# Optimization experiments

Hardware: AMD Instinct MI355X
Metric: run time of the kernel (lower is better)

## Reference

```python
import jax, jax.numpy as jnp
import numpy as np
from jax import lax

DIM = 96
B, S = 2, 48
EPS_LN = 1e-6
EPS_GRN = 1e-6


def setup_inputs() -> dict:
    key = jax.random.key(0)
    ks = jax.random.split(key, 11)
    d, h = DIM, 4 * DIM
    return {
        "x": jax.random.normal(ks[0], (B, d, S, S, S), jnp.float32),
        "dw_w": jax.random.normal(ks[1], (d, 1, 7, 7, 7), jnp.float32) * 0.05,  # (O, I/groups, kD,kH,kW)
        "dw_b": jax.random.normal(ks[2], (d,), jnp.float32) * 0.02,
        "ln_w": jnp.ones((d,), jnp.float32),
        "ln_b": jnp.zeros((d,), jnp.float32),
        "w1": jax.random.normal(ks[3], (d, h), jnp.float32) * 0.02,
        "b1": jax.random.normal(ks[4], (h,), jnp.float32) * 0.02,
        "grn_w": jax.random.normal(ks[5], (h,), jnp.float32) * 0.02,
        "grn_b": jax.random.normal(ks[6], (h,), jnp.float32) * 0.02,
        "w2": jax.random.normal(ks[7], (h, d), jnp.float32) * 0.02,
        "b2": jax.random.normal(ks[8], (d,), jnp.float32) * 0.02,
    }


def reference(x, dw_w, dw_b, ln_w, ln_b, w1, b1, grn_w, grn_b, w2, b2):
    # depthwise 7x7x7 conv, padding 3, groups = channels; x: (B, C, D, H, W)
    y = lax.conv_general_dilated(
        x, dw_w, window_strides=(1, 1, 1), padding=[(3, 3)] * 3,
        dimension_numbers=("NCDHW", "OIDHW", "NCDHW"), feature_group_count=DIM,
    ) + dw_b[None, :, None, None, None]
    # channels_last: (B, D, H, W, C)
    h = jnp.transpose(y, (0, 2, 3, 4, 1))
    # LayerNorm over channel dim
    mu = jnp.mean(h, axis=-1, keepdims=True)
    var = jnp.mean((h - mu) ** 2, axis=-1, keepdims=True)
    h = (h - mu) * lax.rsqrt(var + EPS_LN) * ln_w + ln_b
    # pointwise MLP expand + GELU (exact, erf-based, like torch)
    h = jnp.einsum("bdhwc,ce->bdhwe", h, w1) + b1
    h = jax.nn.gelu(h, approximate=False)
    # GRN: global L2 norm over spatial dims (1,2,3), per channel
    g = jnp.sqrt(jnp.sum(h * h, axis=(1, 2, 3), keepdims=True))  # (B,1,1,1,4C)
    n = g / (jnp.mean(g, axis=-1, keepdims=True) + EPS_GRN)
    h = grn_w * (h * n) + grn_b + h
    # pointwise MLP contract
    h = jnp.einsum("bdhwe,ec->bdhwc", h, w2) + b2
    # back to channels_first + residual
    return x + jnp.transpose(h, (0, 4, 1, 2, 3))
```

## Files before the change

kernel.cpp:

```cpp
#include <hip/hip_runtime.h>
#include <hip/hip_bf16.h>
#include <string.h>

#define S3 110592
#define CDIM 96
#define EDIM 384
#define ZIN 14
#define YIN 22

typedef __attribute__((ext_vector_type(8))) short bf16x8;
typedef __attribute__((ext_vector_type(4))) float f32x4;
typedef unsigned short ushort_t;

__device__ __forceinline__ ushort_t f2bf(float f) {
  __hip_bfloat16 h = __float2bfloat16(f);
  union { __hip_bfloat16 h; ushort_t u; } cv; cv.h = h; return cv.u;
}
__device__ __forceinline__ float bf2f(ushort_t u) {
  union { __hip_bfloat16 h; ushort_t u; } cv; cv.u = u; return __bfloat162float(cv.h);
}
__device__ __forceinline__ float gelu_fast(float v) {
  float u = v * (-1.59576912f - 0.07135481f * v * v);
  float s = __expf(u);
  return __fdividef(v, 1.f + s);
}

__global__ void kprep(const float* __restrict__ ln_w, const float* __restrict__ ln_b,
                      const float* __restrict__ w1, const float* __restrict__ b1,
                      const float* __restrict__ grn_b, const float* __restrict__ w2,
                      const float* __restrict__ b2,
                      ushort_t* __restrict__ w1p, float* __restrict__ b1f, float* __restrict__ bias2) {
  int idx = blockIdx.x * 256 + threadIdx.x;
  if (idx < 24 * 3 * 64 * 8) {
    int j = idx & 7, lane = (idx >> 3) & 63, ks = (idx >> 9) % 3, nt = idx / 1536;
    int c = ks * 32 + (lane >> 4) * 8 + j;
    int e = nt * 16 + (lane & 15);
    w1p[idx] = f2bf(ln_w[c] * w1[c * EDIM + e]);
  }
  if (idx < EDIM) {
    float s = b1[idx];
    for (int c = 0; c < CDIM; ++c) s += ln_b[c] * w1[c * EDIM + idx];
    b1f[idx] = s;
  }
  if (idx < CDIM) {
    float s = b2[idx];
    for (int e = 0; e < EDIM; ++e) s += grn_b[e] * w2[e * CDIM + idx];
    bias2[idx] = s;
  }
}

__global__ void kpackB(const float* __restrict__ dw_w, ushort_t* __restrict__ Btab) {
  int idx = blockIdx.x * 256 + threadIdx.x;
  if (idx >= 96 * 49 * 512) return;
  int pos = idx & 511; int t = (idx >> 9) % 49; int c = idx / (49 * 512);
  int lane = pos >> 3, j = pos & 7;
  int k = (lane >> 4) * 8 + j, n = lane & 15;
  int tx = k - n - 1;
  int tz = t / 7, ty = t % 7;
  float v = (tx >= 0 && tx < 7) ? dw_w[c * 343 + tz * 49 + ty * 7 + tx] : 0.f;
  Btab[idx] = f2bf(v);
}

template<int HALF>
__device__ __forceinline__ void conv_ty_loop(const unsigned* tile, const ushort_t* Bt,
                                             int lane, int am, int xg, f32x4* acc) {
#pragma unroll 1
  for (int ty = 0; ty < 7; ++ty) {
    bf16x8 bfr[7];
#pragma unroll
    for (int tz = 0; tz < 7; ++tz)
      bfr[tz] = *(const bf16x8*)&Bt[(tz * 7 + ty) * 512 + lane * 8];
    int rowbase = am + ty;
#pragma unroll
    for (int zl = 0; zl < 7; ++zl) {
      int row = (HALF * 7 + zl) * YIN + rowbase;
      int byteoff = (row << 7) + (xg ^ ((row & 7) << 4));
      bf16x8 af = *(const bf16x8*)((const char*)tile + byteoff);
#pragma unroll
      for (int tz = 0; tz < 7; ++tz) {
        int l = (HALF == 0) ? (zl - tz) : (zl + 6 - tz);
        if (l >= 0 && l < 7)
          acc[l] = __builtin_amdgcn_mfma_f32_16x16x32_bf16(af, bfr[tz], acc[l], 0, 0, 0);
      }
    }
  }
}

__global__ __launch_bounds__(384, 6) void kconv(const float* __restrict__ x,
                                                const ushort_t* __restrict__ Btab,
                                                const float* __restrict__ dw_b,
                                                ushort_t* __restrict__ y) {
  __shared__ unsigned tile[ZIN * YIN * 32];
  int bid = blockIdx.x;
  int xcd = bid & 7, wi = bid >> 3;
  int c = xcd * 12 + wi / 36;
  int rr_ = wi % 36;
  int b = rr_ / 18;
  int t_ = rr_ % 18;
  int zt = t_ / 3, yt = t_ % 3;
  int z0 = zt * 8, y0 = yt * 16;
  size_t base = (size_t)(b * 96 + c) * S3;
  int tid = threadIdx.x;

  for (int i = tid; i < 308 * 8; i += 384) {
    int row = i >> 3; int pe = i & 7;
    int pc = (pe < 2) ? pe : pe + 24;
    tile[(row << 5) + (pc ^ ((row & 7) << 2))] = 0u;
  }
#pragma unroll 4
  for (int i = tid; i < 308 * 24; i += 384) {
    int row = i / 24; int pc = 2 + (i - row * 24);
    int dz = row / YIN, dy = row - dz * YIN;
    int gz = z0 - 3 + dz, gy = y0 - 3 + dy;
    float2 v = make_float2(0.f, 0.f);
    if ((unsigned)gz < 48u && (unsigned)gy < 48u)
      v = *(const float2*)&x[base + (size_t)gz * 2304 + gy * 48 + 2 * pc - 4];
    tile[(row << 5) + (pc ^ ((row & 7) << 2))] = (unsigned)f2bf(v.x) | ((unsigned)f2bf(v.y) << 16);
  }
  __syncthreads();

  int w = tid >> 6;
  int X = w % 3, half = w / 3;
  int lane = tid & 63;
  int am = lane & 15, g = lane >> 4;
  int xg = X * 32 + g * 16;

  f32x4 acc[7];
#pragma unroll
  for (int p = 0; p < 7; ++p) acc[p] = (f32x4){0.f, 0.f, 0.f, 0.f};

  const ushort_t* __restrict__ Bt = Btab + (size_t)c * 49 * 512;
  if (half == 0) conv_ty_loop<0>(tile, Bt, lane, am, xg, acc);
  else           conv_ty_loop<1>(tile, Bt, lane, am, xg, acc);

  float bv = dw_b[c];
  float* red = (float*)tile;
  int rcol = X * 16 + am;
  __syncthreads();
  if (half == 0) {
#pragma unroll
    for (int l = 1; l < 7; ++l)
#pragma unroll
      for (int r = 0; r < 4; ++r)
        red[(l - 1) * 800 + (g * 4 + r) * 50 + rcol] = acc[l][r];
  }
  __syncthreads();
  if (half == 0) {
    size_t zb = base + (size_t)z0 * 2304;
#pragma unroll
    for (int r = 0; r < 4; ++r)
      y[zb + (size_t)(y0 + g * 4 + r) * 48 + rcol] = f2bf(acc[0][r] + bv);
  } else {
#pragma unroll
    for (int l = 0; l < 7; ++l) {
      size_t zb = base + (size_t)(z0 + l + 1) * 2304;
#pragma unroll
      for (int r = 0; r < 4; ++r) {
        float v = acc[l][r] + bv;
        if (l < 6) v += red[l * 800 + (g * 4 + r) * 50 + rcol];
        y[zb + (size_t)(y0 + g * 4 + r) * 48 + rcol] = f2bf(v);
      }
    }
  }
}

__global__ __launch_bounds__(512, 4) void ksum(const ushort_t* __restrict__ y,
                                               const ushort_t* __restrict__ w1p,
                                               const float* __restrict__ b1f,
                                               float* __restrict__ sumsq) {
  __shared__ ushort_t Al[64 * 104];
  __shared__ float red_s[8][64], red_q[8][64];
  __shared__ float stat_mu[64], stat_rv[64];
  __shared__ float ssq_s[EDIM];
  int tid = threadIdx.x;
  int q = tid >> 6, lane = tid & 63;
  size_t pos0 = (size_t)blockIdx.x * 64;
  int b = (int)(pos0 / S3);
  int sp0 = (int)(pos0 % S3);

  bf16x8 bfg[3][3];
#pragma unroll
  for (int ntl = 0; ntl < 3; ++ntl)
#pragma unroll
    for (int ks = 0; ks < 3; ++ks)
      bfg[ntl][ks] = *(const bf16x8*)&w1p[(size_t)(((q * 3 + ntl) * 3 + ks) * 64 + lane) * 8];

  float v[12];
  float s = 0.f, ss = 0.f;
  const ushort_t* yb = y + (size_t)b * 96 * S3 + sp0 + lane;
#pragma unroll
  for (int i = 0; i < 12; ++i) {
    float f = bf2f(yb[(size_t)(q * 12 + i) * S3]);
    v[i] = f; s += f; ss += f * f;
  }
  red_s[q][lane] = s; red_q[q][lane] = ss;
  __syncthreads();
  if (tid < 64) {
    float su = 0.f, sq = 0.f;
#pragma unroll
    for (int k = 0; k < 8; ++k) { su += red_s[k][tid]; sq += red_q[k][tid]; }
    float mu = su * (1.f / 96.f);
    float var = sq * (1.f / 96.f) - mu * mu;
    stat_mu[tid] = mu;
    stat_rv[tid] = rsqrtf(var + 1e-6f);
  }
  __syncthreads();
  {
    float mu = stat_mu[lane], rv = stat_rv[lane];
#pragma unroll
    for (int i4 = 0; i4 < 3; ++i4) {
      ushort_t u0 = f2bf((v[i4 * 4 + 0] - mu) * rv);
      ushort_t u1 = f2bf((v[i4 * 4 + 1] - mu) * rv);
      ushort_t u2 = f2bf((v[i4 * 4 + 2] - mu) * rv);
      ushort_t u3 = f2bf((v[i4 * 4 + 3] - mu) * rv);
      uint2 t; t.x = (unsigned)u0 | ((unsigned)u1 << 16); t.y = (unsigned)u2 | ((unsigned)u3 << 16);
      *(uint2*)&Al[lane * 104 + q * 12 + i4 * 4] = t;
    }
  }
  __syncthreads();

  f32x4 acc[4][3];
#pragma unroll
  for (int mt = 0; mt < 4; ++mt)
#pragma unroll
    for (int ntl = 0; ntl < 3; ++ntl) acc[mt][ntl] = (f32x4){0.f, 0.f, 0.f, 0.f};

  int row = lane & 15, g = lane >> 4;
#pragma unroll
  for (int ks = 0; ks < 3; ++ks) {
    bf16x8 af[4];
    int colb = ks * 32 + g * 8;
#pragma unroll
    for (int mt = 0; mt < 4; ++mt)
      af[mt] = *(const bf16x8*)&Al[(mt * 16 + row) * 104 + colb];
#pragma unroll
    for (int ntl = 0; ntl < 3; ++ntl) {
#pragma unroll
      for (int mt = 0; mt < 4; ++mt)
        acc[mt][ntl] = __builtin_amdgcn_mfma_f32_16x16x32_bf16(af[mt], bfg[ntl][ks], acc[mt][ntl], 0, 0, 0);
    }
  }

#pragma unroll
  for (int ntl = 0; ntl < 3; ++ntl) {
    int e = q * 48 + ntl * 16 + row;
    float bb = b1f[e];
    float ssq = 0.f;
#pragma unroll
    for (int mt = 0; mt < 4; ++mt) {
#pragma unroll
      for (int r = 0; r < 4; ++r) {
        float gel = gelu_fast(acc[mt][ntl][r] + bb);
        ssq += gel * gel;
      }
    }
    ssq += __shfl_xor(ssq, 16, 64);
    ssq += __shfl_xor(ssq, 32, 64);
    if (g == 0) ssq_s[e] = ssq;
  }
  __syncthreads();
  if (tid < EDIM) atomicAdd(&sumsq[b * EDIM + tid], ssq_s[tid]);
}

__global__ void kscale(const float* __restrict__ sumsq, const float* __restrict__ grn_w,
                       float* __restrict__ scale) {
  __shared__ float wsum[6];
  __shared__ float mean_s;
  int b = blockIdx.x, e = threadIdx.x;
  float gv = sqrtf(sumsq[b * EDIM + e]);
  float t = gv;
#pragma unroll
  for (int off = 1; off <= 32; off <<= 1) t += __shfl_xor(t, off, 64);
  if ((e & 63) == 0) wsum[e >> 6] = t;
  __syncthreads();
  if (e == 0) {
    float m = 0.f;
    for (int i = 0; i < 6; ++i) m += wsum[i];
    mean_s = m * (1.f / EDIM);
  }
  __syncthreads();
  scale[b * EDIM + e] = grn_w[e] * (gv / (mean_s + 1e-6f)) + 1.f;
}

__global__ void kpackw2(const float* __restrict__ scale, const float* __restrict__ w2,
                        ushort_t* __restrict__ w2s) {
  int idx = blockIdx.x * 256 + threadIdx.x;
  int b = idx / 36864; int r = idx % 36864;
  int j = r & 7, lane = (r >> 3) & 63, ks = (r >> 9) % 12, nt = r / 6144;
  int e = ks * 32 + (lane >> 4) * 8 + j, cc = nt * 16 + (lane & 15);
  w2s[idx] = f2bf(scale[b * EDIM + e] * w2[e * CDIM + cc]);
}

__global__ __launch_bounds__(512, 4) void kfused(const ushort_t* __restrict__ y,
                                                 const ushort_t* __restrict__ w1p,
                                                 const float* __restrict__ b1f,
                                                 const ushort_t* __restrict__ w2s,
                                                 const float* __restrict__ bias2,
                                                 const float* __restrict__ x,
                                                 float* __restrict__ out) {
  __shared__ __align__(16) char smem[68096];
  ushort_t* Al   = (ushort_t*)smem;
  float* red_s   = (float*)(smem + 13312);
  float* red_q   = (float*)(smem + 15360);
  float* stat_mu = (float*)(smem + 17408);
  float* stat_rv = (float*)(smem + 17664);
  ushort_t* htile= (ushort_t*)(smem + 17920);
  float* otile   = (float*)(smem + 17920);

  int tid = threadIdx.x;
  int q = tid >> 6, lane = tid & 63;
  size_t pos0 = (size_t)blockIdx.x * 64;
  int b = (int)(pos0 / S3);
  int sp0 = (int)(pos0 % S3);
  int row = lane & 15, g = lane >> 4;

  float v[12];
  float s = 0.f, ss = 0.f;
  const ushort_t* yb = y + (size_t)b * 96 * S3 + sp0 + lane;
#pragma unroll
  for (int i = 0; i < 12; ++i) {
    float f = bf2f(yb[(size_t)(q * 12 + i) * S3]);
    v[i] = f; s += f; ss += f * f;
  }
  red_s[q * 64 + lane] = s; red_q[q * 64 + lane] = ss;
  __syncthreads();
  if (tid < 64) {
    float su = 0.f, sq = 0.f;
#pragma unroll
    for (int k = 0; k < 8; ++k) { su += red_s[k * 64 + tid]; sq += red_q[k * 64 + tid]; }
    float mu = su * (1.f / 96.f);
    float var = sq * (1.f / 96.f) - mu * mu;
    stat_mu[tid] = mu;
    stat_rv[tid] = rsqrtf(var + 1e-6f);
  }
  __syncthreads();
  {
    float mu = stat_mu[lane], rv = stat_rv[lane];
#pragma unroll
    for (int i4 = 0; i4 < 3; ++i4) {
      ushort_t u0 = f2bf((v[i4 * 4 + 0] - mu) * rv);
      ushort_t u1 = f2bf((v[i4 * 4 + 1] - mu) * rv);
      ushort_t u2 = f2bf((v[i4 * 4 + 2] - mu) * rv);
      ushort_t u3 = f2bf((v[i4 * 4 + 3] - mu) * rv);
      uint2 t; t.x = (unsigned)u0 | ((unsigned)u1 << 16); t.y = (unsigned)u2 | ((unsigned)u3 << 16);
      *(uint2*)&Al[lane * 104 + q * 12 + i4 * 4] = t;
    }
  }
  __syncthreads();

  f32x4 acc[4][3];
#pragma unroll
  for (int mt = 0; mt < 4; ++mt)
#pragma unroll
    for (int ntl = 0; ntl < 3; ++ntl) acc[mt][ntl] = (f32x4){0.f, 0.f, 0.f, 0.f};

#pragma unroll
  for (int ks = 0; ks < 3; ++ks) {
    bf16x8 af[4];
    int colb = ks * 32 + g * 8;
#pragma unroll
    for (int mt = 0; mt < 4; ++mt)
      af[mt] = *(const bf16x8*)&Al[(mt * 16 + row) * 104 + colb];
#pragma unroll
    for (int ntl = 0; ntl < 3; ++ntl) {
      bf16x8 bfg = *(const bf16x8*)&w1p[(size_t)(((q * 3 + ntl) * 3 + ks) * 64 + lane) * 8];
#pragma unroll
      for (int mt = 0; mt < 4; ++mt)
        acc[mt][ntl] = __builtin_amdgcn_mfma_f32_16x16x32_bf16(af[mt], bfg, acc[mt][ntl], 0, 0, 0);
    }
  }

#pragma unroll
  for (int ntl = 0; ntl < 3; ++ntl) {
    int e = q * 48 + ntl * 16 + row;
    float bb = b1f[e];
#pragma unroll
    for (int mt = 0; mt < 4; ++mt) {
#pragma unroll
      for (int r = 0; r < 4; ++r) {
        float gel = gelu_fast(acc[mt][ntl][r] + bb);
        htile[(mt * 16 + g * 4 + r) * 392 + e] = f2bf(gel);
      }
    }
  }
  __syncthreads();

  int mt2 = q & 3, nh = q >> 2;
  f32x4 acc2[3];
#pragma unroll
  for (int ntl = 0; ntl < 3; ++ntl) acc2[ntl] = (f32x4){0.f, 0.f, 0.f, 0.f};
  const ushort_t* w2b = w2s + (size_t)b * 36864;
  const ushort_t* arow = &htile[(mt2 * 16 + row) * 392];
#pragma unroll
  for (int ks = 0; ks < 12; ++ks) {
    bf16x8 af2 = *(const bf16x8*)&arow[g * 8 + ks * 32];
#pragma unroll
    for (int ntl = 0; ntl < 3; ++ntl) {
      int nt = nh * 3 + ntl;
      bf16x8 bfg2 = *(const bf16x8*)&w2b[(size_t)((nt * 12 + ks) * 64 + lane) * 8];
      acc2[ntl] = __builtin_amdgcn_mfma_f32_16x16x32_bf16(af2, bfg2, acc2[ntl], 0, 0, 0);
    }
  }
  __syncthreads();

#pragma unroll
  for (int ntl = 0; ntl < 3; ++ntl) {
    int cc = (nh * 3 + ntl) * 16 + row;
#pragma unroll
    for (int r = 0; r < 4; ++r)
      otile[cc * 65 + mt2 * 16 + g * 4 + r] = acc2[ntl][r];
  }
  __syncthreads();

#pragma unroll
  for (int k = 0; k < 6; ++k) {
    int idx = tid + k * 512;
    int cc = idx >> 5, pp = (idx & 31) * 2;
    size_t o = (size_t)(b * 96 + cc) * S3 + sp0 + pp;
    float2 xv = *(const float2*)&x[o];
    float bb = bias2[cc];
    float2 ov;
    ov.x = xv.x + otile[cc * 65 + pp] + bb;
    ov.y = xv.y + otile[cc * 65 + pp + 1] + bb;
    *(float2*)&out[o] = ov;
  }
}

extern "C" void kernel_launch(void* const* d_in, const int* in_sizes, int n_in,
                              void* d_out, int out_size, void* d_ws, size_t ws_size,
                              hipStream_t stream) {
  const float* x     = (const float*)d_in[0];
  const float* dw_w  = (const float*)d_in[1];
  const float* dw_b  = (const float*)d_in[2];
  const float* ln_w  = (const float*)d_in[3];
  const float* ln_b  = (const float*)d_in[4];
  const float* w1    = (const float*)d_in[5];
  const float* b1    = (const float*)d_in[6];
  const float* grn_w = (const float*)d_in[7];
  const float* grn_b = (const float*)d_in[8];
  const float* w2    = (const float*)d_in[9];
  const float* b2    = (const float*)d_in[10];
  float* out = (float*)d_out;

  char* ws = (char*)d_ws;
  size_t off = 0;
  auto alloc = [&](size_t bytes) -> void* {
    void* p = ws + off;
    off = (off + bytes + 511) & ~(size_t)511;
    return p;
  };
  ushort_t* y    = (ushort_t*)alloc((size_t)2 * 96 * S3 * 2);
  ushort_t* w1p  = (ushort_t*)alloc(36864 * 2);
  ushort_t* w2s  = (ushort_t*)alloc((size_t)2 * 36864 * 2);
  ushort_t* Btab = (ushort_t*)alloc((size_t)96 * 49 * 512 * 2);
  float* b1f     = (float*)alloc(EDIM * 4);
  float* bias2   = (float*)alloc(CDIM * 4);
  float* sumsq   = (float*)alloc(2 * EDIM * 4);
  float* scale   = (float*)alloc(2 * EDIM * 4);

  hipMemsetAsync(sumsq, 0, 2 * EDIM * 4, stream);
  kprep<<<145, 256, 0, stream>>>(ln_w, ln_b, w1, b1, grn_b, w2, b2, w1p, b1f, bias2);
  kpackB<<<9408, 256, 0, stream>>>(dw_w, Btab);
  kconv<<<3456, 384, 0, stream>>>(x, Btab, dw_b, y);
  ksum<<<3456, 512, 0, stream>>>(y, w1p, b1f, sumsq);
  kscale<<<2, 384, 0, stream>>>(sumsq, grn_w, scale);
  kpackw2<<<288, 256, 0, stream>>>(scale, w2, w2s);
  kfused<<<3456, 512, 0, stream>>>(y, w1p, b1f, w2s, bias2, x, out);
}
```

Measured before the change: 307.2 us.

## Store normalized bf16 activations in ksum and reuse them in kfused

ksum now writes the LayerNorm-normalized bf16 activation tile (position-major, 96 channels) to a new workspace buffer. kfused reads that buffer directly instead of reloading y in strided channel-major form and recomputing the LayerNorm statistics, which removes two barriers and the reduction. kfused also switches to 32-position tiles with 256 threads and a smaller LDS footprint so more blocks fit per CU. The cost is about 42MB of extra global writes in ksum and the same amount read back in kfused, and each wave now reads its A fragments straight from global memory.

Measured after the change: 323.7 us. +5.4%, slower.

```diff
diff --git a/kernel.cpp b/kernel.cpp
--- a/kernel.cpp
+++ b/kernel.cpp
@@ -167,7 +167,8 @@
 __global__ __launch_bounds__(512, 4) void ksum(const ushort_t* __restrict__ y,
                                                const ushort_t* __restrict__ w1p,
                                                const float* __restrict__ b1f,
-                                               float* __restrict__ sumsq) {
+                                               float* __restrict__ sumsq,
+                                               ushort_t* __restrict__ anorm) {
   __shared__ ushort_t Al[64 * 104];
   __shared__ float red_s[8][64], red_q[8][64];
   __shared__ float stat_mu[64], stat_rv[64];
@@ -219,6 +220,14 @@
   }
   __syncthreads();
 
+  {
+    uint4* dst = (uint4*)(anorm + pos0 * 96);
+    for (int i = tid; i < 64 * 12; i += 512) {
+      int p = i / 12, j = i - p * 12;
+      dst[p * 12 + j] = *(const uint4*)&Al[p * 104 + j * 8];
+    }
+  }
+
   f32x4 acc[4][3];
 #pragma unroll
   for (int mt = 0; mt < 4; ++mt)
@@ -291,91 +300,53 @@
   w2s[idx] = f2bf(scale[b * EDIM + e] * w2[e * CDIM + cc]);
 }
 
-__global__ __launch_bounds__(512, 4) void kfused(const ushort_t* __restrict__ y,
+__global__ __launch_bounds__(256, 5) void kfused(const ushort_t* __restrict__ anorm,
                                                  const ushort_t* __restrict__ w1p,
                                                  const float* __restrict__ b1f,
                                                  const ushort_t* __restrict__ w2s,
                                                  const float* __restrict__ bias2,
                                                  const float* __restrict__ x,
                                                  float* __restrict__ out) {
-  __shared__ __align__(16) char smem[68096];
-  ushort_t* Al   = (ushort_t*)smem;
-  float* red_s   = (float*)(smem + 13312);
-  float* red_q   = (float*)(smem + 15360);
-  float* stat_mu = (float*)(smem + 17408);
-  float* stat_rv = (float*)(smem + 17664);
-  ushort_t* htile= (ushort_t*)(smem + 17920);
-  float* otile   = (float*)(smem + 17920);
+  __shared__ __align__(16) char smem[32 * 392 * 2];
+  ushort_t* htile = (ushort_t*)smem;
+  float* otile    = (float*)smem;
 
   int tid = threadIdx.x;
   int q = tid >> 6, lane = tid & 63;
-  size_t pos0 = (size_t)blockIdx.x * 64;
+  size_t pos0 = (size_t)blockIdx.x * 32;
   int b = (int)(pos0 / S3);
   int sp0 = (int)(pos0 % S3);
   int row = lane & 15, g = lane >> 4;
 
-  float v[12];
-  float s = 0.f, ss = 0.f;
-  const ushort_t* yb = y + (size_t)b * 96 * S3 + sp0 + lane;
-#pragma unroll
-  for (int i = 0; i < 12; ++i) {
-    float f = bf2f(yb[(size_t)(q * 12 + i) * S3]);
-    v[i] = f; s += f; ss += f * f;
-  }
-  red_s[q * 64 + lane] = s; red_q[q * 64 + lane] = ss;
-  __syncthreads();
-  if (tid < 64) {
-    float su = 0.f, sq = 0.f;
-#pragma unroll
-    for (int k = 0; k < 8; ++k) { su += red_s[k * 64 + tid]; sq += red_q[k * 64 + tid]; }
-    float mu = su * (1.f / 96.f);
-    float var = sq * (1.f / 96.f) - mu * mu;
-    stat_mu[tid] = mu;
-    stat_rv[tid] = rsqrtf(var + 1e-6f);
-  }
-  __syncthreads();
-  {
-    float mu = stat_mu[lane], rv = stat_rv[lane];
-#pragma unroll
-    for (int i4 = 0; i4 < 3; ++i4) {
-      ushort_t u0 = f2bf((v[i4 * 4 + 0] - mu) * rv);
-      ushort_t u1 = f2bf((v[i4 * 4 + 1] - mu) * rv);
-      ushort_t u2 = f2bf((v[i4 * 4 + 2] - mu) * rv);
-      ushort_t u3 = f2bf((v[i4 * 4 + 3] - mu) * rv);
-      uint2 t; t.x = (unsigned)u0 | ((unsigned)u1 << 16); t.y = (unsigned)u2 | ((unsigned)u3 << 16);
-      *(uint2*)&Al[lane * 104 + q * 12 + i4 * 4] = t;
-    }
-  }
-  __syncthreads();
-
-  f32x4 acc[4][3];
-#pragma unroll
-  for (int mt = 0; mt < 4; ++mt)
-#pragma unroll
-    for (int ntl = 0; ntl < 3; ++ntl) acc[mt][ntl] = (f32x4){0.f, 0.f, 0.f, 0.f};
-
+  f32x4 acc[2][6];
+#pragma unroll
+  for (int mt = 0; mt < 2; ++mt)
+#pragma unroll
+    for (int ntl = 0; ntl < 6; ++ntl) acc[mt][ntl] = (f32x4){0.f, 0.f, 0.f, 0.f};
+
+  const ushort_t* ab = anorm + pos0 * 96;
 #pragma unroll
   for (int ks = 0; ks < 3; ++ks) {
-    bf16x8 af[4];
     int colb = ks * 32 + g * 8;
-#pragma unroll
-    for (int mt = 0; mt < 4; ++mt)
-      af[mt] = *(const bf16x8*)&Al[(mt * 16 + row) * 104 + colb];
-#pragma unroll
-    for (int ntl = 0; ntl < 3; ++ntl) {
-      bf16x8 bfg = *(const bf16x8*)&w1p[(size_t)(((q * 3 + ntl) * 3 + ks) * 64 + lane) * 8];
-#pragma unroll
-      for (int mt = 0; mt < 4; ++mt)
+    bf16x8 af[2];
+#pragma unroll
+    for (int mt = 0; mt < 2; ++mt)
+      af[mt] = *(const bf16x8*)&ab[(mt * 16 + row) * 96 + colb];
+#pragma unroll
+    for (int ntl = 0; ntl < 6; ++ntl) {
+      bf16x8 bfg = *(const bf16x8*)&w1p[(size_t)(((q * 6 + ntl) * 3 + ks) * 64 + lane) * 8];
+#pragma unroll
+      for (int mt = 0; mt < 2; ++mt)
         acc[mt][ntl] = __builtin_amdgcn_mfma_f32_16x16x32_bf16(af[mt], bfg, acc[mt][ntl], 0, 0, 0);
     }
   }
 
 #pragma unroll
-  for (int ntl = 0; ntl < 3; ++ntl) {
-    int e = q * 48 + ntl * 16 + row;
+  for (int ntl = 0; ntl < 6; ++ntl) {
+    int e = q * 96 + ntl * 16 + row;
     float bb = b1f[e];
 #pragma unroll
-    for (int mt = 0; mt < 4; ++mt) {
+    for (int mt = 0; mt < 2; ++mt) {
 #pragma unroll
       for (int r = 0; r < 4; ++r) {
         float gel = gelu_fast(acc[mt][ntl][r] + bb);
@@ -385,7 +356,7 @@
   }
   __syncthreads();
 
-  int mt2 = q & 3, nh = q >> 2;
+  int mt2 = q & 1, nh = q >> 1;
   f32x4 acc2[3];
 #pragma unroll
   for (int ntl = 0; ntl < 3; ++ntl) acc2[ntl] = (f32x4){0.f, 0.f, 0.f, 0.f};
@@ -408,20 +379,20 @@
     int cc = (nh * 3 + ntl) * 16 + row;
 #pragma unroll
     for (int r = 0; r < 4; ++r)
-      otile[cc * 65 + mt2 * 16 + g * 4 + r] = acc2[ntl][r];
+      otile[cc * 33 + mt2 * 16 + g * 4 + r] = acc2[ntl][r];
   }
   __syncthreads();
 
 #pragma unroll
   for (int k = 0; k < 6; ++k) {
-    int idx = tid + k * 512;
-    int cc = idx >> 5, pp = (idx & 31) * 2;
+    int idx = tid + k * 256;
+    int cc = idx >> 4, pp = (idx & 15) * 2;
     size_t o = (size_t)(b * 96 + cc) * S3 + sp0 + pp;
     float2 xv = *(const float2*)&x[o];
     float bb = bias2[cc];
     float2 ov;
-    ov.x = xv.x + otile[cc * 65 + pp] + bb;
-    ov.y = xv.y + otile[cc * 65 + pp + 1] + bb;
+    ov.x = xv.x + otile[cc * 33 + pp] + bb;
+    ov.y = xv.y + otile[cc * 33 + pp + 1] + bb;
     *(float2*)&out[o] = ov;
   }
 }
@@ -449,21 +420,22 @@
     off = (off + bytes + 511) & ~(size_t)511;
     return p;
   };
-  ushort_t* y    = (ushort_t*)alloc((size_t)2 * 96 * S3 * 2);
-  ushort_t* w1p  = (ushort_t*)alloc(36864 * 2);
-  ushort_t* w2s  = (ushort_t*)alloc((size_t)2 * 36864 * 2);
-  ushort_t* Btab = (ushort_t*)alloc((size_t)96 * 49 * 512 * 2);
-  float* b1f     = (float*)alloc(EDIM * 4);
-  float* bias2   = (float*)alloc(CDIM * 4);
-  float* sumsq   = (float*)alloc(2 * EDIM * 4);
-  float* scale   = (float*)alloc(2 * EDIM * 4);
+  ushort_t* y     = (ushort_t*)alloc((size_t)2 * 96 * S3 * 2);
+  ushort_t* anorm = (ushort_t*)alloc((size_t)221184 * 96 * 2);
+  ushort_t* w1p   = (ushort_t*)alloc(36864 * 2);
+  ushort_t* w2s   = (ushort_t*)alloc((size_t)2 * 36864 * 2);
+  ushort_t* Btab  = (ushort_t*)alloc((size_t)96 * 49 * 512 * 2);
+  float* b1f      = (float*)alloc(EDIM * 4);
+  float* bias2    = (float*)alloc(CDIM * 4);
+  float* sumsq    = (float*)alloc(2 * EDIM * 4);
+  float* scale    = (float*)alloc(2 * EDIM * 4);
 
   hipMemsetAsync(sumsq, 0, 2 * EDIM * 4, stream);
   kprep<<<145, 256, 0, stream>>>(ln_w, ln_b, w1, b1, grn_b, w2, b2, w1p, b1f, bias2);
   kpackB<<<9408, 256, 0, stream>>>(dw_w, Btab);
   kconv<<<3456, 384, 0, stream>>>(x, Btab, dw_b, y);
-  ksum<<<3456, 512, 0, stream>>>(y, w1p, b1f, sumsq);
+  ksum<<<3456, 512, 0, stream>>>(y, w1p, b1f, sumsq, anorm);
   kscale<<<2, 384, 0, stream>>>(sumsq, grn_w, scale);
   kpackw2<<<288, 256, 0, stream>>>(scale, w2, w2s);
-  kfused<<<3456, 512, 0, stream>>>(y, w1p, b1f, w2s, bias2, x, out);
-}
+  kfused<<<6912, 256, 0, stream>>>(anorm, w1p, b1f, w2s, bias2, x, out);
+}
```
